# Kernel tuning notes

Measured on AMD Instinct MI355X. Metric: run time of the kernel, lower is better.

## Reference

```python
import jax, jax.numpy as jnp
import numpy as np

B, S, D, H = 2, 2048, 1024, 16
DH = D // H  # 64


def setup_inputs() -> dict:
    key = jax.random.key(0)
    ks = jax.random.split(key, 12)
    inp = {
        "hidden_states": jax.random.normal(ks[0], (B, S, D), dtype=jnp.float32),
        "attention_mask": jax.random.randint(ks[1], (B, S), 0, 2, dtype=jnp.int32),
        "Wq": jax.random.normal(ks[2], (D, D), dtype=jnp.float32) / np.sqrt(D),
        "bq": jnp.zeros((D,), dtype=jnp.float32),
        "Wk": jax.random.normal(ks[3], (D, D), dtype=jnp.float32) / np.sqrt(D),
        "bk": jnp.zeros((D,), dtype=jnp.float32),
        "Wv": jax.random.normal(ks[4], (D, D), dtype=jnp.float32) / np.sqrt(D),
        "bv": jnp.zeros((D,), dtype=jnp.float32),
        # per-head additive query bias (emotion manipulation path)
        "emotion_w": jax.random.normal(ks[5], (H, DH), dtype=jnp.float32),
        "Wo": jax.random.normal(ks[6], (D, D), dtype=jnp.float32) / np.sqrt(D),
        "bo": jnp.zeros((D,), dtype=jnp.float32),
    }
    return inp


def reference(hidden_states, attention_mask, Wq, bq, Wk, bk, Wv, bv, emotion_w, Wo, bo):
    b, s, d = hidden_states.shape
    # projections -> [b, h, s, dh]
    def proj(W, bias):
        y = hidden_states @ W + bias
        return y.reshape(b, s, H, DH).transpose(0, 2, 1, 3)

    q = proj(Wq, bq)
    k = proj(Wk, bk)
    v = proj(Wv, bv)

    # manipulation_type='emotion': additive per-head query bias
    q = q + emotion_w[None, :, None, :]

    scores = jnp.einsum("bhqd,bhkd->bhqk", q, k) / np.sqrt(DH).astype(np.float32)
    # key-padding mask: positions where mask==0 get -inf
    scores = jnp.where(attention_mask[:, None, None, :] == 0, -jnp.inf, scores)
    attn = jax.nn.softmax(scores, axis=-1)  # dropout is identity in eval mode

    out = jnp.einsum("bhqk,bhkd->bhqd", attn, v)
    out = out.transpose(0, 2, 1, 3).reshape(b, s, d)
    return out @ Wo + bo
```

## Files before the change

kernel.cpp:

```cpp
#include <hip/hip_runtime.h>
#include <hip/hip_bf16.h>


#define B_  2
#define S_  2048
#define D_  1024
#define K_  1024
#define H_  16
#define DH_ 64
#define BS_ (B_*S_)

typedef __hip_bfloat16 bf16;
typedef __attribute__((ext_vector_type(8))) short s8v;
typedef __attribute__((ext_vector_type(4))) short s4v;
typedef __attribute__((ext_vector_type(4))) float f4v;

__device__ __forceinline__ float b2f(bf16 x) { return __bfloat162float(x); }
__device__ __forceinline__ bf16  f2b(float x) { return __float2bfloat16(x); }

__device__ __forceinline__ void gl_lds_16B(const bf16* g, bf16* l) {
    __builtin_amdgcn_global_load_lds(
        (const __attribute__((address_space(1))) unsigned int*)g,
        (__attribute__((address_space(3))) unsigned int*)l, 16, 0, 0);
}

#define QSCALE_ 0.1803368801f

__global__ __launch_bounds__(256) void convert_x_kernel(
    const float* __restrict__ X, bf16* __restrict__ Xb)
{
    const size_t idx = ((size_t)blockIdx.x * 256 + threadIdx.x) * 4;
    const float4 v = *(const float4*)(X + idx);
    bf16 t0 = f2b(v.x), t1 = f2b(v.y), t2 = f2b(v.z), t3 = f2b(v.w);
    s4v o;
    o[0] = *(short*)&t0; o[1] = *(short*)&t1;
    o[2] = *(short*)&t2; o[3] = *(short*)&t3;
    *(s4v*)(Xb + idx) = o;
}

__global__ __launch_bounds__(256) void convert_mask_kernel(
    const int* __restrict__ mask, bf16* __restrict__ mkbf)
{
    const int idx = blockIdx.x * 256 + threadIdx.x;
    mkbf[idx] = f2b(mask[idx] ? 1.0f : 0.0f);
}

__global__ __launch_bounds__(256) void transpose_w_kernel(
    const float* __restrict__ Wq, const float* __restrict__ Wk,
    const float* __restrict__ Wv, const float* __restrict__ Wo,
    bf16* __restrict__ WTq, bf16* __restrict__ WTk,
    bf16* __restrict__ WTv, bf16* __restrict__ WTo)
{
    const int z = blockIdx.z;
    const float* __restrict__ W = (z == 0) ? Wq : (z == 1) ? Wk : (z == 2) ? Wv : Wo;
    bf16* __restrict__ WT       = (z == 0) ? WTq : (z == 1) ? WTk : (z == 2) ? WTv : WTo;

    const int k0 = blockIdx.x * 64;
    const int n0 = blockIdx.y * 64;

    __shared__ float Ls[64][68];

    const int t  = threadIdx.x;
    const int lr = t >> 4;
    const int lc = (t & 15) * 4;

    #pragma unroll
    for (int i = 0; i < 4; i++) {
        const int k = i * 16 + lr;
        const float4 v = *(const float4*)(W + (size_t)(k0 + k) * K_ + n0 + lc);
        Ls[k][lc + 0] = v.x; Ls[k][lc + 1] = v.y;
        Ls[k][lc + 2] = v.z; Ls[k][lc + 3] = v.w;
    }
    __syncthreads();
    #pragma unroll
    for (int i = 0; i < 4; i++) {
        const int n = i * 16 + lr;
        s4v o;
        #pragma unroll
        for (int j = 0; j < 4; j++) {
            bf16 tb = f2b(Ls[lc + j][n]);
            o[j] = *(short*)&tb;
        }
        *(s4v*)(WT + (size_t)(n0 + n) * K_ + k0 + lc) = o;
    }
}

template <bool SWAPPED>
__device__ __forceinline__ void gemm_tile(
    const bf16* __restrict__ A, const bf16* __restrict__ BT,
    int m0, int n0, bf16* As, bf16* Bs, f4v acc[4][4])
{
    const int t    = threadIdx.x;
    const int lane = t & 63;
    const int wave = t >> 6;
    const int quad = lane >> 4;
    const int l15  = lane & 15;
    const int wr   = wave >> 1;
    const int wc   = wave & 1;

    const int sr = t >> 3;
    const int sc = (t & 7) * 8;

    for (int kb = 0; kb < K_; kb += 64) {
        #pragma unroll
        for (int i = 0; i < 4; i++) {
            const int r = i * 32 + sr;
            gl_lds_16B(A  + (size_t)(m0 + r) * K_ + kb + sc, As + r * 64 + sc);
            gl_lds_16B(BT + (size_t)(n0 + r) * K_ + kb + sc, Bs + r * 64 + sc);
        }
        __syncthreads();

        #pragma unroll
        for (int ks = 0; ks < 2; ks++) {
            s8v fA[4], fB[4];
            #pragma unroll
            for (int i = 0; i < 4; i++) {
                fA[i] = *(const s8v*)&As[(wr * 64 + i * 16 + l15) * 64 + ks * 32 + quad * 8];
                fB[i] = *(const s8v*)&Bs[(wc * 64 + i * 16 + l15) * 64 + ks * 32 + quad * 8];
            }
            #pragma unroll
            for (int i = 0; i < 4; i++)
                #pragma unroll
                for (int j = 0; j < 4; j++)
                    acc[i][j] = SWAPPED
                        ? __builtin_amdgcn_mfma_f32_16x16x32_bf16(fB[i], fA[j], acc[i][j], 0, 0, 0)
                        : __builtin_amdgcn_mfma_f32_16x16x32_bf16(fA[i], fB[j], acc[i][j], 0, 0, 0);
        }
        __syncthreads();
    }
}

__global__ __launch_bounds__(256) void proj_qkv_kernel(
    const bf16* __restrict__ Xb,
    const bf16* __restrict__ WTq, const float* __restrict__ bq,
    const bf16* __restrict__ WTk, const float* __restrict__ bk,
    const bf16* __restrict__ WTv, const float* __restrict__ bv,
    const float* __restrict__ emo, const int* __restrict__ mask,
    bf16* __restrict__ q_ws, bf16* __restrict__ k_ws, bf16* __restrict__ v_ws)
{
    const int m0 = blockIdx.x * 128;
    const int n0 = blockIdx.y * 128;
    const int z  = blockIdx.z;

    __shared__ __align__(16) bf16 As[128 * 64];
    __shared__ __align__(16) bf16 Bs[128 * 64];

    const int t    = threadIdx.x;
    const int lane = t & 63;
    const int wave = t >> 6;
    const int quad = lane >> 4;
    const int l15  = lane & 15;
    const int wr   = wave >> 1;
    const int wc   = wave & 1;

    f4v acc[4][4] = {};

    if (z == 0) {
        gemm_tile<false>(Xb, WTq, m0, n0, As, Bs, acc);
        #pragma unroll
        for (int j = 0; j < 4; j++) {
            const int n  = n0 + wc * 64 + j * 16 + l15;
            const int h  = n >> 6, dh = n & 63;
            const float bias_n = bq[n] + emo[n];
            #pragma unroll
            for (int i = 0; i < 4; i++) {
                #pragma unroll
                for (int r = 0; r < 4; r++) {
                    const int m = m0 + wr * 64 + i * 16 + quad * 4 + r;
                    const int b = m >> 11, s = m & 2047;
                    q_ws[(((size_t)(b * H_ + h)) * S_ + s) * DH_ + dh] =
                        f2b((acc[i][j][r] + bias_n) * QSCALE_);
                }
            }
        }
    } else if (z == 1) {
        gemm_tile<false>(Xb, WTk, m0, n0, As, Bs, acc);
        #pragma unroll
        for (int j = 0; j < 4; j++) {
            const int n  = n0 + wc * 64 + j * 16 + l15;
            const int h  = n >> 6, dh = n & 63;
            const float bias_n = bk[n];
            #pragma unroll
            for (int i = 0; i < 4; i++) {
                #pragma unroll
                for (int r = 0; r < 4; r++) {
                    const int m = m0 + wr * 64 + i * 16 + quad * 4 + r;
                    const int b = m >> 11, s = m & 2047;
                    k_ws[(((size_t)(b * H_ + h)) * S_ + s) * DH_ + dh] =
                        f2b(acc[i][j][r] + bias_n);
                }
            }
        }
    } else {
        gemm_tile<true>(Xb, WTv, m0, n0, As, Bs, acc);
        #pragma unroll
        for (int j = 0; j < 4; j++) {
            const int m = m0 + wr * 64 + j * 16 + l15;
            const int b = m >> 11, s = m & 2047;
            const float msk = mask[b * S_ + s] ? 1.0f : 0.0f;
            #pragma unroll
            for (int i = 0; i < 4; i++) {
                #pragma unroll
                for (int r = 0; r < 4; r++) {
                    const int n  = n0 + wc * 64 + i * 16 + quad * 4 + r;
                    const int h  = n >> 6, dh = n & 63;
                    v_ws[(((size_t)(b * H_ + h)) * DH_ + dh) * S_ + s] =
                        f2b((acc[i][j][r] + bv[n]) * msk);
                }
            }
        }
    }
}

__global__ __launch_bounds__(256) void proj_out_kernel(
    const bf16* __restrict__ ctx, const bf16* __restrict__ WTo,
    const float* __restrict__ bo, float* __restrict__ out)
{
    const int m0 = blockIdx.x * 64;
    const int n0 = blockIdx.y * 128;

    __shared__ __align__(16) bf16 As[64 * 64];
    __shared__ __align__(16) bf16 Bs[128 * 64];

    const int t    = threadIdx.x;
    const int lane = t & 63;
    const int wave = t >> 6;
    const int quad = lane >> 4;
    const int l15  = lane & 15;
    const int wr   = wave >> 1;
    const int wc   = wave & 1;

    const int sr = t >> 3;
    const int sc = (t & 7) * 8;

    f4v acc[2][4] = {};

    for (int kb = 0; kb < K_; kb += 64) {
        #pragma unroll
        for (int i = 0; i < 2; i++) {
            const int r = i * 32 + sr;
            gl_lds_16B(ctx + (size_t)(m0 + r) * K_ + kb + sc, As + r * 64 + sc);
        }
        #pragma unroll
        for (int i = 0; i < 4; i++) {
            const int r = i * 32 + sr;
            gl_lds_16B(WTo + (size_t)(n0 + r) * K_ + kb + sc, Bs + r * 64 + sc);
        }
        __syncthreads();

        #pragma unroll
        for (int ks = 0; ks < 2; ks++) {
            s8v fA[2], fB[4];
            #pragma unroll
            for (int i = 0; i < 2; i++)
                fA[i] = *(const s8v*)&As[(wr * 32 + i * 16 + l15) * 64 + ks * 32 + quad * 8];
            #pragma unroll
            for (int j = 0; j < 4; j++)
                fB[j] = *(const s8v*)&Bs[(wc * 64 + j * 16 + l15) * 64 + ks * 32 + quad * 8];
            #pragma unroll
            for (int i = 0; i < 2; i++)
                #pragma unroll
                for (int j = 0; j < 4; j++)
                    acc[i][j] = __builtin_amdgcn_mfma_f32_16x16x32_bf16(fA[i], fB[j], acc[i][j], 0, 0, 0);
        }
        __syncthreads();
    }

    #pragma unroll
    for (int j = 0; j < 4; j++) {
        const int n = n0 + wc * 64 + j * 16 + l15;
        const float bias_n = bo[n];
        #pragma unroll
        for (int i = 0; i < 2; i++) {
            #pragma unroll
            for (int r = 0; r < 4; r++) {
                const int m = m0 + wr * 32 + i * 16 + quad * 4 + r;
                out[(size_t)m * D_ + n] = acc[i][j][r] + bias_n;
            }
        }
    }
}

#define PP_ 88

__global__ __launch_bounds__(256) void attn_kernel(
    const bf16* __restrict__ q_ws, const bf16* __restrict__ k_ws,
    const bf16* __restrict__ v_ws, const bf16* __restrict__ mkbf,
    bf16* __restrict__ ctx)
{
    const int bh = blockIdx.x;
    const int q0 = blockIdx.y * 64;
    const int b  = bh >> 4;
    const int h  = bh & 15;

    __shared__ __align__(16) bf16 k_lds[64 * 64];
    __shared__ __align__(16) bf16 vt_lds[64 * 64];
    __shared__ __align__(16) bf16 p_lds[4][16 * PP_];

    const int t    = threadIdx.x;
    const int wave = t >> 6;
    const int lane = t & 63;
    const int quad = lane >> 4;
    const int l15  = lane & 15;
    const int lxor = l15 & 7;

    s8v qf[2];
    #pragma unroll
    for (int dt = 0; dt < 2; dt++)
        qf[dt] = *(const s8v*)(q_ws +
            ((size_t)bh * S_ + q0 + wave * 16 + l15) * DH_ + dt * 32 + quad * 8);

    f4v oacc[4] = {};
    f4v osum   = {};

    int srw[2], scs[2];
    #pragma unroll
    for (int c = 0; c < 2; c++) {
        const int e = c * 2048 + t * 8;
        srw[c] = e >> 6;
        scs[c] = ((e >> 3) & 7) ^ (srw[c] & 7);
    }

    for (int kb0 = 0; kb0 < S_; kb0 += 64) {
        #pragma unroll
        for (int c = 0; c < 2; c++) {
            const int e = c * 2048 + t * 8;
            const int r = srw[c], cs = scs[c];
            gl_lds_16B(k_ws + ((size_t)bh * S_ + kb0) * DH_ + r * 64 + cs * 8,
                       k_lds + e);
            gl_lds_16B(v_ws + ((size_t)bh * DH_ + r) * S_ + kb0 + cs * 8,
                       vt_lds + e);
        }
        __syncthreads();

        f4v sacc[4] = {};
        #pragma unroll
        for (int kt = 0; kt < 4; kt++) {
            #pragma unroll
            for (int dt = 0; dt < 2; dt++) {
                const s8v kf = *(const s8v*)&k_lds[(kt * 16 + l15) * 64 +
                                                   ((dt * 4 + quad) ^ lxor) * 8];
                sacc[kt] = __builtin_amdgcn_mfma_f32_16x16x32_bf16(kf, qf[dt], sacc[kt], 0, 0, 0);
            }
        }

        #pragma unroll
        for (int kt = 0; kt < 4; kt++) {
            float2 e01, e23;
            e01.x = exp2f(sacc[kt][0]);
            e01.y = exp2f(sacc[kt][1]);
            e23.x = exp2f(sacc[kt][2]);
            e23.y = exp2f(sacc[kt][3]);
            union { __hip_bfloat162 h; unsigned u; } lo, hi;
            lo.h = __float22bfloat162_rn(e01);
            hi.h = __float22bfloat162_rn(e23);
            *(uint2*)&p_lds[wave][l15 * PP_ + kt * 16 + quad * 4] =
                make_uint2(lo.u, hi.u);
        }

        __builtin_amdgcn_s_waitcnt(0xC07F);

        #pragma unroll
        for (int kh = 0; kh < 2; kh++) {
            const s8v ap = *(const s8v*)&p_lds[wave][l15 * PP_ + kh * 32 + quad * 8];
            const s8v mv = *(const s8v*)(mkbf + (size_t)b * S_ + kb0 + kh * 32 + quad * 8);
            #pragma unroll
            for (int nt = 0; nt < 4; nt++) {
                const s8v vf = *(const s8v*)&vt_lds[(nt * 16 + l15) * 64 +
                                                    ((kh * 4 + quad) ^ lxor) * 8];
                oacc[nt] = __builtin_amdgcn_mfma_f32_16x16x32_bf16(ap, vf, oacc[nt], 0, 0, 0);
            }
            osum = __builtin_amdgcn_mfma_f32_16x16x32_bf16(ap, mv, osum, 0, 0, 0);
        }
        __syncthreads();
    }

    #pragma unroll
    for (int r = 0; r < 4; r++) {
        const float inv = 1.0f / osum[r];
        const int q = q0 + wave * 16 + quad * 4 + r;
        #pragma unroll
        for (int nt = 0; nt < 4; nt++)
            ctx[((size_t)b * S_ + q) * D_ + h * DH_ + nt * 16 + l15] =
                f2b(oacc[nt][r] * inv);
    }
}

extern "C" void kernel_launch(void* const* d_in, const int* in_sizes, int n_in,
                              void* d_out, int out_size, void* d_ws, size_t ws_size,
                              hipStream_t stream) {
    (void)in_sizes; (void)n_in; (void)out_size; (void)ws_size;

    const float* X    = (const float*)d_in[0];
    const int*   mask = (const int*)d_in[1];
    const float* Wq   = (const float*)d_in[2];
    const float* bq   = (const float*)d_in[3];
    const float* Wk   = (const float*)d_in[4];
    const float* bk   = (const float*)d_in[5];
    const float* Wv   = (const float*)d_in[6];
    const float* bv   = (const float*)d_in[7];
    const float* emo  = (const float*)d_in[8];
    const float* Wo   = (const float*)d_in[9];
    const float* bo   = (const float*)d_in[10];
    float* out = (float*)d_out;

    bf16* q_ws = (bf16*)d_ws;
    bf16* k_ws = q_ws + (size_t)BS_ * D_;
    bf16* v_ws = k_ws + (size_t)BS_ * D_;
    bf16* ctx  = v_ws + (size_t)BS_ * D_;
    bf16* Xb   = ctx  + (size_t)BS_ * D_;
    bf16* WTq  = Xb   + (size_t)BS_ * D_;
    bf16* WTk  = WTq  + (size_t)D_ * K_;
    bf16* WTv  = WTk  + (size_t)D_ * K_;
    bf16* WTo  = WTv  + (size_t)D_ * K_;
    bf16* mkbf = WTo  + (size_t)D_ * K_;

    hipLaunchKernelGGL(convert_x_kernel, dim3(BS_ * D_ / 1024), dim3(256), 0, stream, X, Xb);
    hipLaunchKernelGGL(convert_mask_kernel, dim3(BS_ / 256), dim3(256), 0, stream, mask, mkbf);
    hipLaunchKernelGGL(transpose_w_kernel, dim3(K_ / 64, D_ / 64, 4), dim3(256), 0, stream,
                       Wq, Wk, Wv, Wo, WTq, WTk, WTv, WTo);
    hipLaunchKernelGGL(proj_qkv_kernel, dim3(BS_ / 128, D_ / 128, 3), dim3(256), 0, stream,
                       Xb, WTq, bq, WTk, bk, WTv, bv, emo, mask, q_ws, k_ws, v_ws);
    hipLaunchKernelGGL(attn_kernel, dim3(B_ * H_, S_ / 64), dim3(256), 0, stream,
                       q_ws, k_ws, v_ws, mkbf, ctx);
    hipLaunchKernelGGL(proj_out_kernel, dim3(BS_ / 64, D_ / 128), dim3(256), 0, stream,
                       ctx, WTo, bo, out);
}
```

Measured before the change: 233.3 us.

## Double-buffer K/V tiles in LDS and stage key mask in shared memory

```diff
diff --git a/kernel.cpp b/kernel.cpp
--- a/kernel.cpp
+++ b/kernel.cpp
@@ -293,9 +293,10 @@
     const int b  = bh >> 4;
     const int h  = bh & 15;
 
-    __shared__ __align__(16) bf16 k_lds[64 * 64];
-    __shared__ __align__(16) bf16 vt_lds[64 * 64];
+    __shared__ __align__(16) bf16 k_lds[2][64 * 64];
+    __shared__ __align__(16) bf16 vt_lds[2][64 * 64];
     __shared__ __align__(16) bf16 p_lds[4][16 * PP_];
+    __shared__ __align__(16) bf16 mk_lds[S_];
 
     const int t    = threadIdx.x;
     const int wave = t >> 6;
@@ -313,33 +314,47 @@
     f4v oacc[4] = {};
     f4v osum   = {};
 
-    int srw[2], scs[2];
+    const bf16* kbase = k_ws + (size_t)bh * S_ * DH_;
+    const bf16* vbase = v_ws + (size_t)bh * DH_ * S_;
+    int off_l[2], off_k[2], off_v[2];
     #pragma unroll
     for (int c = 0; c < 2; c++) {
         const int e = c * 2048 + t * 8;
-        srw[c] = e >> 6;
-        scs[c] = ((e >> 3) & 7) ^ (srw[c] & 7);
-    }
-
-    for (int kb0 = 0; kb0 < S_; kb0 += 64) {
-        #pragma unroll
-        for (int c = 0; c < 2; c++) {
-            const int e = c * 2048 + t * 8;
-            const int r = srw[c], cs = scs[c];
-            gl_lds_16B(k_ws + ((size_t)bh * S_ + kb0) * DH_ + r * 64 + cs * 8,
-                       k_lds + e);
-            gl_lds_16B(v_ws + ((size_t)bh * DH_ + r) * S_ + kb0 + cs * 8,
-                       vt_lds + e);
-        }
+        const int r = e >> 6;
+        const int cs = ((e >> 3) & 7) ^ (r & 7);
+        off_l[c] = e;
+        off_k[c] = r * 64 + cs * 8;
+        off_v[c] = r * S_ + cs * 8;
+    }
+
+    gl_lds_16B(mkbf + (size_t)b * S_ + t * 8, mk_lds + t * 8);
+    #pragma unroll
+    for (int c = 0; c < 2; c++) {
+        gl_lds_16B(kbase + off_k[c], &k_lds[0][off_l[c]]);
+        gl_lds_16B(vbase + off_v[c], &vt_lds[0][off_l[c]]);
+    }
+
+    for (int it = 0; it < S_ / 64; it++) {
+        const int cur = it & 1;
         __syncthreads();
 
+        if (it + 1 < S_ / 64) {
+            const int nk = (it + 1) * 4096;
+            const int nv = (it + 1) * 64;
+            #pragma unroll
+            for (int c = 0; c < 2; c++) {
+                gl_lds_16B(kbase + nk + off_k[c], &k_lds[cur ^ 1][off_l[c]]);
+                gl_lds_16B(vbase + nv + off_v[c], &vt_lds[cur ^ 1][off_l[c]]);
+            }
+        }
+
         f4v sacc[4] = {};
         #pragma unroll
         for (int kt = 0; kt < 4; kt++) {
             #pragma unroll
             for (int dt = 0; dt < 2; dt++) {
-                const s8v kf = *(const s8v*)&k_lds[(kt * 16 + l15) * 64 +
-                                                   ((dt * 4 + quad) ^ lxor) * 8];
+                const s8v kf = *(const s8v*)&k_lds[cur][(kt * 16 + l15) * 64 +
+                                                        ((dt * 4 + quad) ^ lxor) * 8];
                 sacc[kt] = __builtin_amdgcn_mfma_f32_16x16x32_bf16(kf, qf[dt], sacc[kt], 0, 0, 0);
             }
         }
@@ -351,9 +366,9 @@
             e01.y = exp2f(sacc[kt][1]);
             e23.x = exp2f(sacc[kt][2]);
             e23.y = exp2f(sacc[kt][3]);
-            union { __hip_bfloat162 h; unsigned u; } lo, hi;
-            lo.h = __float22bfloat162_rn(e01);
-            hi.h = __float22bfloat162_rn(e23);
+            union { __hip_bfloat162 hh; unsigned u; } lo, hi;
+            lo.hh = __float22bfloat162_rn(e01);
+            hi.hh = __float22bfloat162_rn(e23);
             *(uint2*)&p_lds[wave][l15 * PP_ + kt * 16 + quad * 4] =
                 make_uint2(lo.u, hi.u);
         }
@@ -363,16 +378,15 @@
         #pragma unroll
         for (int kh = 0; kh < 2; kh++) {
             const s8v ap = *(const s8v*)&p_lds[wave][l15 * PP_ + kh * 32 + quad * 8];
-            const s8v mv = *(const s8v*)(mkbf + (size_t)b * S_ + kb0 + kh * 32 + quad * 8);
+            const s8v mv = *(const s8v*)&mk_lds[it * 64 + kh * 32 + quad * 8];
             #pragma unroll
             for (int nt = 0; nt < 4; nt++) {
-                const s8v vf = *(const s8v*)&vt_lds[(nt * 16 + l15) * 64 +
-                                                    ((kh * 4 + quad) ^ lxor) * 8];
+                const s8v vf = *(const s8v*)&vt_lds[cur][(nt * 16 + l15) * 64 +
+                                                         ((kh * 4 + quad) ^ lxor) * 8];
                 oacc[nt] = __builtin_amdgcn_mfma_f32_16x16x32_bf16(ap, vf, oacc[nt], 0, 0, 0);
             }
             osum = __builtin_amdgcn_mfma_f32_16x16x32_bf16(ap, mv, osum, 0, 0, 0);
         }
-        __syncthreads();
     }
 
     #pragma unroll
```

Result: slower. 248.1 us (+6.4%).
